# Optimization experiments

Hardware: AMD Instinct MI355X
Metric: run time of the kernel (lower is better)

Reference implementation:

```python
import jax, jax.numpy as jnp
import numpy as np
from jax import lax

B, CIN, IMG, K = 128, 3, 112, 7
C = 1024      # hidden_channels * channel_dilation
HID = 512     # hidden_channels
HW = (IMG // K) ** 2  # 256 patches
EPS = 1e-5


def _prelu(x, a):
    return jnp.where(x > 0, x, a * x)


def _bn(x, g, b):
    # BatchNorm2d with track_running_stats=False: always uses batch stats
    m = x.mean(axis=(0, 2, 3), keepdims=True)
    v = x.var(axis=(0, 2, 3), keepdims=True)
    return (x - m) * lax.rsqrt(v + EPS) * g[None, :, None, None] + b[None, :, None, None]


def setup_inputs() -> dict:
    key = jax.random.key(0)
    ks = jax.random.split(key, 16)
    d = {
        'x':  jax.random.normal(ks[0], (B, CIN, IMG, IMG), jnp.float32),
        'w0': jax.random.normal(ks[1], (C, CIN, K, K), jnp.float32) * 0.05,
        'b0': jax.random.normal(ks[2], (C,), jnp.float32) * 0.01,
        'a0': jnp.full((1,), 0.25, jnp.float32),
    }
    for i in range(1, 4):
        kw, kb = jax.random.split(jax.random.fold_in(key, i))
        d[f'w{i}'] = jax.random.normal(kw, (C, C), jnp.float32) * 0.02
        d[f'b{i}'] = jax.random.normal(kb, (C,), jnp.float32) * 0.01
        d[f'g{i}'] = jnp.ones((C,), jnp.float32)
        d[f'bt{i}'] = jnp.zeros((C,), jnp.float32)
        d[f'p{i}'] = jnp.full((1,), 0.25, jnp.float32)
    d['pos'] = jax.random.normal(ks[3], (1, HW, C), jnp.float32)
    d['am'] = jnp.full((1,), 0.25, jnp.float32)
    d['wm'] = jax.random.normal(ks[4], (HID, C), jnp.float32) * 0.03
    d['bm'] = jax.random.normal(ks[5], (HID,), jnp.float32) * 0.01
    pkeys = jax.random.split(ks[6], B)
    d['perm'] = jax.vmap(lambda k: jax.random.permutation(k, HW))(pkeys).astype(jnp.int32)
    return d


def reference(x, w0, b0, a0,
              w1, b1, g1, bt1, p1,
              w2, b2, g2, bt2, p2,
              w3, b3, g3, bt3, p3,
              pos, am, wm, bm, perm):
    # patch-embed conv: stride = kernel_size -> [B, C, 16, 16]
    h = lax.conv_general_dilated(x, w0, (K, K), 'VALID',
                                 dimension_numbers=('NCHW', 'OIHW', 'NCHW'))
    h = _prelu(h + b0[None, :, None, None], a0)
    for w, b, g, bt, p in ((w1, b1, g1, bt1, p1),
                           (w2, b2, g2, bt2, p2),
                           (w3, b3, g3, bt3, p3)):
        h = jnp.einsum('bchw,dc->bdhw', h, w) + b[None, :, None, None]  # 1x1 conv
        h = _prelu(_bn(h, g, bt), p)
    Bn, Cn, Hn, Wn = h.shape
    enc = h.reshape(Bn, Cn, Hn * Wn).transpose(0, 2, 1)  # [B, HW, C]
    enc = enc + pos                                      # private: add pos embedding
    enc = _prelu(enc, am) @ wm.T + bm                    # mixer -> [B, HW, HID]
    # private: per-sample token permutation (single batched gather)
    return jnp.take_along_axis(enc, perm[:, :, None], axis=1)
```

## Files before the change

kernel.cpp:

```cpp
#include <hip/hip_runtime.h>
#include <hip/hip_bf16.h>
#include <stdint.h>


typedef __attribute__((ext_vector_type(8))) short bf16x8;
typedef __attribute__((ext_vector_type(4))) float f32x4;

__device__ __forceinline__ float bf2f(uint32_t u) {
  union { uint32_t i; float f; } v; v.i = u << 16; return v.f;
}
__device__ __forceinline__ ushort f2bf(float f) {
  union { float f; uint32_t i; } v; v.f = f;
  uint32_t i = v.i;
  return (ushort)((i + 0x7FFFu + ((i >> 16) & 1u)) >> 16);
}

template<int EPI, int XB, int K, int DOUT>
__global__ void __launch_bounds__(512, 2)
gemm_kernel(const ushort* __restrict__ A, const ushort* __restrict__ Bw,
            const float* __restrict__ bias, const float* __restrict__ alpha,
            void* __restrict__ outp, float* __restrict__ part,
            const int* __restrict__ inv)
{
  __shared__ __align__(16) ushort At[2][256 * 64];
  __shared__ __align__(16) ushort Bt[2][256 * 64];
  const int tid  = threadIdx.x;
  const int lane = tid & 63;
  const int wid  = tid >> 6;
  const int wm   = wid >> 2;
  const int wn   = wid & 3;

  const int s = blockIdx.x;
  const int j = s >> 3;
  const int x = j & ((1 << XB) - 1);
  const int y = ((j >> XB) << 3) | (s & 7);
  const int t0 = y << 8;
  const int d0 = x << 8;

  f32x4 acc[8][4] = {};

  const int swz = (((lane >> 4) ^ (lane & 7)) << 4);
  const char* LA0 = (const char*)&At[0][0] + ((((wm << 7) + (lane & 15))) << 7) + swz;
  const char* LA1 = (const char*)&At[0][0] + ((((wm << 7) + (lane & 15))) << 7) + (swz ^ 64);
  const char* LB0 = (const char*)&Bt[0][0] + ((((wn << 6) + (lane & 15))) << 7) + swz;
  const char* LB1 = (const char*)&Bt[0][0] + ((((wn << 6) + (lane & 15))) << 7) + (swz ^ 64);

  const int lrow8 = lane >> 3;
  const int csrc  = (lane & 7) ^ lrow8;
  const ushort* gAw = A  + (size_t)(t0 + (wid << 4) + lrow8) * K + (csrc << 3);
  const ushort* gBw = Bw + (size_t)(d0 + (wid << 4) + lrow8) * K + (csrc << 3);
  char* stA = (char*)&At[0][0] + (wid << 11);
  char* stB = (char*)&Bt[0][0] + (wid << 11);

#define STAGE_A(T, BUF, H) do {                                                          \
    __builtin_amdgcn_global_load_lds(                                                    \
      (const __attribute__((address_space(1))) uint32_t*)(gAw + (size_t)((H)*128)*K + ((size_t)(T) << 6)),     \
      (__attribute__((address_space(3))) uint32_t*)(stA + (BUF)*32768 + (H)*16384), 16, 0, 0);                  \
    __builtin_amdgcn_global_load_lds(                                                    \
      (const __attribute__((address_space(1))) uint32_t*)(gAw + (size_t)((H)*128+8)*K + ((size_t)(T) << 6)),   \
      (__attribute__((address_space(3))) uint32_t*)(stA + (BUF)*32768 + (H)*16384 + 1024), 16, 0, 0);           \
  } while (0)
#define STAGE_B(T, BUF, H) do {                                                          \
    __builtin_amdgcn_global_load_lds(                                                    \
      (const __attribute__((address_space(1))) uint32_t*)(gBw + (size_t)((H)*128)*K + ((size_t)(T) << 6)),     \
      (__attribute__((address_space(3))) uint32_t*)(stB + (BUF)*32768 + (H)*16384), 16, 0, 0);                  \
    __builtin_amdgcn_global_load_lds(                                                    \
      (const __attribute__((address_space(1))) uint32_t*)(gBw + (size_t)((H)*128+8)*K + ((size_t)(T) << 6)),   \
      (__attribute__((address_space(3))) uint32_t*)(stB + (BUF)*32768 + (H)*16384 + 1024), 16, 0, 0);           \
  } while (0)

#define RD_A(dst, BASE, CUR, MH) do {                                                    \
    dst[0] = *(const bf16x8*)((BASE) + (CUR)*32768 + (MH)*8192 + 0);                     \
    dst[1] = *(const bf16x8*)((BASE) + (CUR)*32768 + (MH)*8192 + 2048);                  \
    dst[2] = *(const bf16x8*)((BASE) + (CUR)*32768 + (MH)*8192 + 4096);                  \
    dst[3] = *(const bf16x8*)((BASE) + (CUR)*32768 + (MH)*8192 + 6144);                  \
  } while (0)
#define RD_B(dst, BASE, CUR) do {                                                        \
    dst[0] = *(const bf16x8*)((BASE) + (CUR)*32768 + 0);                                 \
    dst[1] = *(const bf16x8*)((BASE) + (CUR)*32768 + 2048);                              \
    dst[2] = *(const bf16x8*)((BASE) + (CUR)*32768 + 4096);                              \
    dst[3] = *(const bf16x8*)((BASE) + (CUR)*32768 + 6144);                              \
  } while (0)
#define MFMA16(AF, BF, MH) do {                                                          \
    __builtin_amdgcn_s_setprio(1);                                                       \
    _Pragma("unroll")                                                                    \
    for (int m_ = 0; m_ < 4; ++m_)                                                       \
      _Pragma("unroll")                                                                  \
      for (int n_ = 0; n_ < 4; ++n_)                                                     \
        acc[((MH) << 2) + m_][n_] = __builtin_amdgcn_mfma_f32_16x16x32_bf16(             \
            AF[m_], BF[n_], acc[((MH) << 2) + m_][n_], 0, 0, 0);                         \
    __builtin_amdgcn_s_setprio(0);                                                       \
  } while (0)

#define TILE_BODY(T, CUR, HN1, HN2) do {                                                 \
                         \
    if (HN1) { asm volatile("s_waitcnt vmcnt(4)" ::: "memory"); }                        \
    else     { asm volatile("s_waitcnt vmcnt(0)" ::: "memory"); }                        \
    __builtin_amdgcn_s_barrier();                                                        \
                 \
    RD_B(b0f, LB0, CUR);                                                                 \
    RD_B(b1f, LB1, CUR);                                                                 \
    RD_A(aX, LA0, CUR, 0);                                                               \
    RD_A(aY, LA0, CUR, 1);                                                               \
    if (HN1) { STAGE_A((T) + 1, (CUR) ^ 1, 0); STAGE_A((T) + 1, (CUR) ^ 1, 1); }         \
    MFMA16(aX, b0f, 0);                                                                  \
    MFMA16(aY, b0f, 1);                                                                  \
                      \
    __builtin_amdgcn_s_barrier();                                                        \
                                                                           \
    if (HN2) { STAGE_B((T) + 2, CUR, 0); STAGE_B((T) + 2, CUR, 1); }                     \
    RD_A(aX, LA1, CUR, 0);                                                               \
    RD_A(aY, LA1, CUR, 1);                                                               \
    MFMA16(aX, b1f, 0);                                                                  \
    MFMA16(aY, b1f, 1);                                                                  \
  } while (0)

  constexpr int NT = K >> 6;

  STAGE_A(0, 0, 0); STAGE_A(0, 0, 1);
  STAGE_B(0, 0, 0); STAGE_B(0, 0, 1);
  STAGE_B(1, 1, 0); STAGE_B(1, 1, 1);

  bf16x8 aX[4], aY[4], b0f[4], b1f[4];

#pragma unroll 1
  for (int tp = 0; tp < NT; tp += 2) {
    const bool m1 = (tp + 2 < NT);
    TILE_BODY(tp,     0, true, m1);
    TILE_BODY(tp + 1, 1, m1, m1);
  }

  float bs[4];
#pragma unroll
  for (int n = 0; n < 4; ++n) bs[n] = bias[d0 + (wn << 6) + (n << 4) + (lane & 15)];
  float a0v = (EPI == 0) ? alpha[0] : 0.0f;
  float sA[4] = {0.f, 0.f, 0.f, 0.f}, s2A[4] = {0.f, 0.f, 0.f, 0.f};

#pragma unroll
  for (int m = 0; m < 8; ++m) {
#pragma unroll
    for (int r = 0; r < 4; ++r) {
      int row = t0 + (wm << 7) + (m << 4) + ((lane >> 4) << 2) + r;
      int orow = (EPI == 2) ? ((row & ~255) | inv[row]) : row;
#pragma unroll
      for (int n = 0; n < 4; ++n) {
        int d = d0 + (wn << 6) + (n << 4) + (lane & 15);
        float v = acc[m][n][r] + bs[n];
        if (EPI == 0) v = v > 0.f ? v : a0v * v;
        if (EPI == 1) { sA[n] += v; s2A[n] += v * v; }
        if (EPI == 2) ((float*)outp)[(size_t)orow * DOUT + d] = v;
        else          ((ushort*)outp)[(size_t)row * DOUT + d] = f2bf(v);
      }
    }
  }

  if (EPI == 1) {
    float2* sm = (float2*)&At[0][0];
    int slot = (wm << 2) | (lane >> 4);
    __syncthreads();
#pragma unroll
    for (int n = 0; n < 4; ++n) {
      int c = (wn << 6) + (n << 4) + (lane & 15);
      sm[slot * 256 + c] = make_float2(sA[n], s2A[n]);
    }
    __syncthreads();
    if (tid < 256) {
      float ss = 0.f, ss2 = 0.f;
      for (int q = 0; q < 8; ++q) {
        float2 v = sm[q * 256 + tid];
        ss += v.x; ss2 += v.y;
      }
      part[(size_t)y * 2048 + d0 + tid]        = ss;
      part[(size_t)y * 2048 + 1024 + d0 + tid] = ss2;
    }
  }
#undef STAGE_A
#undef STAGE_B
#undef RD_A
#undef RD_B
#undef MFMA16
#undef TILE_BODY
}

__global__ void bnfold_kernel(const float* __restrict__ part, const float* __restrict__ g,
                              const float* __restrict__ bt, float* __restrict__ scsh) {
  int d = (blockIdx.x << 8) + threadIdx.x;
  float s = 0.f, s2 = 0.f;
  for (int j = 0; j < 128; ++j) { s += part[j * 2048 + d]; s2 += part[j * 2048 + 1024 + d]; }
  float mean = s * (1.f / 32768.f);
  float var  = s2 * (1.f / 32768.f) - mean * mean;
  float sc = g[d] * rsqrtf(var + 1e-5f);
  scsh[d] = sc;
  scsh[1024 + d] = bt[d] - mean * sc;
}

template<bool MIX>
__global__ void bnact_kernel(ushort* __restrict__ Y, const float* __restrict__ scsh,
                             const float* __restrict__ p, const float* __restrict__ pos,
                             const float* __restrict__ am) {
  float pp = p[0];
  float aa = MIX ? am[0] : 0.f;
#pragma unroll 1
  for (int it = 0; it < 8; ++it) {
    size_t vi = ((size_t)it << 19) + ((size_t)blockIdx.x << 8) + threadIdx.x;
    size_t i = vi << 3;
    int d = (int)(i & 1023);
    float pv[8];
    if (MIX) {
      int prow = (int)((i >> 10) & 255);
      const float4* pb = (const float4*)(pos + ((size_t)prow << 10) + d);
      float4 pA = pb[0], pB = pb[1];
      pv[0]=pA.x; pv[1]=pA.y; pv[2]=pA.z; pv[3]=pA.w;
      pv[4]=pB.x; pv[5]=pB.y; pv[6]=pB.z; pv[7]=pB.w;
    }
    uint4 raw = *(const uint4*)(Y + i);
    uint32_t w[4] = {raw.x, raw.y, raw.z, raw.w};
    uint32_t o[4];
#pragma unroll
    for (int q = 0; q < 4; ++q) {
      int dd = d + q * 2;
      float v0 = bf2f(w[q] & 0xFFFFu) * scsh[dd]     + scsh[1024 + dd];
      float v1 = bf2f(w[q] >> 16)     * scsh[dd + 1] + scsh[1024 + dd + 1];
      v0 = v0 > 0.f ? v0 : pp * v0;
      v1 = v1 > 0.f ? v1 : pp * v1;
      if (MIX) {
        v0 += pv[2 * q];     v1 += pv[2 * q + 1];
        v0 = v0 > 0.f ? v0 : aa * v0;
        v1 = v1 > 0.f ? v1 : aa * v1;
      }
      o[q] = (uint32_t)f2bf(v0) | ((uint32_t)f2bf(v1) << 16);
    }
    *(uint4*)(Y + i) = make_uint4(o[0], o[1], o[2], o[3]);
  }
}

__global__ void prep_kernel(const float* __restrict__ x,
                            const float* __restrict__ w0, const float* __restrict__ w1,
                            const float* __restrict__ w2, const float* __restrict__ w3,
                            const float* __restrict__ wm, const int* __restrict__ perm,
                            ushort* __restrict__ P, ushort* __restrict__ w0b,
                            ushort* __restrict__ w1b, ushort* __restrict__ w2b,
                            ushort* __restrict__ w3b, ushort* __restrict__ wmb,
                            int* __restrict__ inv) {
  const int b = blockIdx.x, tid = threadIdx.x;
  if (b < 2048) {
    int t0 = b << 4;
#pragma unroll 1
    for (int tt = 0; tt < 16; ++tt) {
      int t = t0 + tt;
      ushort v = 0;
      if (tid < 147) {
        int bb = t >> 8, pidx = t & 255;
        int pi = pidx >> 4, pj = pidx & 15;
        int cin = tid / 49, rem = tid - cin * 49;
        int dy = rem / 7, dx = rem - dy * 7;
        v = f2bf(x[(size_t)(bb * 3 + cin) * 12544 + (size_t)(pi * 7 + dy) * 112 + (pj * 7 + dx)]);
      }
      P[(size_t)t * 256 + tid] = v;
    }
  } else if (b < 4096) {
    int i = ((b - 2048) << 8) + tid;
#pragma unroll
    for (int r = 0; r < 2; ++r) {
      int idx = (r << 19) + i;
      w1b[idx] = f2bf(w1[idx]);
      w2b[idx] = f2bf(w2[idx]);
      w3b[idx] = f2bf(w3[idx]);
    }
    wmb[i] = f2bf(wm[i]);
  } else if (b < 4224) {
    int t = ((b - 4096) << 8) + tid;
    inv[(t & ~255) + perm[t]] = t & 255;
  } else {
    int d = b - 4224;
    w0b[d * 256 + tid] = (tid < 147) ? f2bf(w0[d * 147 + tid]) : (ushort)0;
  }
}

extern "C" void kernel_launch(void* const* d_in, const int* in_sizes, int n_in,
                              void* d_out, int out_size, void* d_ws, size_t ws_size,
                              hipStream_t stream) {
  const float* x   = (const float*)d_in[0];
  const float* w0  = (const float*)d_in[1];
  const float* b0  = (const float*)d_in[2];
  const float* a0  = (const float*)d_in[3];
  const float* w1  = (const float*)d_in[4];
  const float* b1  = (const float*)d_in[5];
  const float* g1  = (const float*)d_in[6];
  const float* bt1 = (const float*)d_in[7];
  const float* p1  = (const float*)d_in[8];
  const float* w2  = (const float*)d_in[9];
  const float* b2  = (const float*)d_in[10];
  const float* g2  = (const float*)d_in[11];
  const float* bt2 = (const float*)d_in[12];
  const float* p2  = (const float*)d_in[13];
  const float* w3  = (const float*)d_in[14];
  const float* b3  = (const float*)d_in[15];
  const float* g3  = (const float*)d_in[16];
  const float* bt3 = (const float*)d_in[17];
  const float* p3  = (const float*)d_in[18];
  const float* pos = (const float*)d_in[19];
  const float* am  = (const float*)d_in[20];
  const float* wm  = (const float*)d_in[21];
  const float* bm  = (const float*)d_in[22];
  const int*  perm = (const int*)d_in[23];

  char* ws = (char*)d_ws;
  ushort* B0   = (ushort*)ws;
  ushort* B1   = (ushort*)(ws + 67108864);
  float*  part = (float*)(ws + 134217728);
  float*  scsh = (float*)(ws + 134217728 + 2097152);
  int*    inv  = (int*)  (ws + 134217728 + 2097152 + 8192);
  char*   wb   = ws + 134217728 + 2097152 + 8192 + 131072;
  ushort* w1b  = (ushort*)wb;
  ushort* w2b  = w1b + 1048576;
  ushort* w3b  = w2b + 1048576;
  ushort* wmb  = w3b + 1048576;
  ushort* w0b  = wmb + 524288;

  prep_kernel<<<dim3(5248), dim3(256), 0, stream>>>(
      x, w0, w1, w2, w3, wm, perm, B1, w0b, w1b, w2b, w3b, wmb, inv);

  gemm_kernel<0, 2, 256, 1024><<<dim3(512), dim3(512), 0, stream>>>(
      B1, w0b, b0, a0, (void*)B0, nullptr, nullptr);

  gemm_kernel<1, 2, 1024, 1024><<<dim3(512), dim3(512), 0, stream>>>(
      B0, w1b, b1, nullptr, (void*)B1, part, nullptr);
  bnfold_kernel<<<dim3(4), dim3(256), 0, stream>>>(part, g1, bt1, scsh);
  bnact_kernel<false><<<dim3(2048), dim3(256), 0, stream>>>(B1, scsh, p1, nullptr, nullptr);

  gemm_kernel<1, 2, 1024, 1024><<<dim3(512), dim3(512), 0, stream>>>(
      B1, w2b, b2, nullptr, (void*)B0, part, nullptr);
  bnfold_kernel<<<dim3(4), dim3(256), 0, stream>>>(part, g2, bt2, scsh);
  bnact_kernel<false><<<dim3(2048), dim3(256), 0, stream>>>(B0, scsh, p2, nullptr, nullptr);

  gemm_kernel<1, 2, 1024, 1024><<<dim3(512), dim3(512), 0, stream>>>(
      B0, w3b, b3, nullptr, (void*)B1, part, nullptr);
  bnfold_kernel<<<dim3(4), dim3(256), 0, stream>>>(part, g3, bt3, scsh);
  bnact_kernel<true><<<dim3(2048), dim3(256), 0, stream>>>(B1, scsh, p3, pos, am);

  gemm_kernel<2, 1, 1024, 512><<<dim3(256), dim3(512), 0, stream>>>(
      B1, wmb, bm, nullptr, d_out, nullptr, inv);
}
```

Measured before the change: 396.3 us.

## Triple-buffer B tiles in LDS to drop the mid-tile barrier

Adds a third LDS buffer for the B operand and rotates read, next and stage indices, so B for tile T+2 can be staged right after the single barrier instead of behind a second one. The wait becomes a full vmcnt(0) at each tile start, and A and B fragment reads are interleaved with the MFMAs. LDS use per block grows from 128 KB to 160 KB, which may limit occupancy (launch bounds ask for 2 blocks per CU). Waiting on all loads each tile may also expose more memory latency.

```diff
diff --git a/kernel.cpp b/kernel.cpp
--- a/kernel.cpp
+++ b/kernel.cpp
@@ -23,7 +23,7 @@
             const int* __restrict__ inv)
 {
   __shared__ __align__(16) ushort At[2][256 * 64];
-  __shared__ __align__(16) ushort Bt[2][256 * 64];
+  __shared__ __align__(16) ushort Bt[3][256 * 64];
   const int tid  = threadIdx.x;
   const int lane = tid & 63;
   const int wid  = tid >> 6;
@@ -60,13 +60,13 @@
       (const __attribute__((address_space(1))) uint32_t*)(gAw + (size_t)((H)*128+8)*K + ((size_t)(T) << 6)),   \
       (__attribute__((address_space(3))) uint32_t*)(stA + (BUF)*32768 + (H)*16384 + 1024), 16, 0, 0);           \
   } while (0)
-#define STAGE_B(T, BUF, H) do {                                                          \
+#define STAGE_B(T, BOFF, H) do {                                                         \
     __builtin_amdgcn_global_load_lds(                                                    \
       (const __attribute__((address_space(1))) uint32_t*)(gBw + (size_t)((H)*128)*K + ((size_t)(T) << 6)),     \
-      (__attribute__((address_space(3))) uint32_t*)(stB + (BUF)*32768 + (H)*16384), 16, 0, 0);                  \
+      (__attribute__((address_space(3))) uint32_t*)(stB + (BOFF) + (H)*16384), 16, 0, 0);                       \
     __builtin_amdgcn_global_load_lds(                                                    \
       (const __attribute__((address_space(1))) uint32_t*)(gBw + (size_t)((H)*128+8)*K + ((size_t)(T) << 6)),   \
-      (__attribute__((address_space(3))) uint32_t*)(stB + (BUF)*32768 + (H)*16384 + 1024), 16, 0, 0);           \
+      (__attribute__((address_space(3))) uint32_t*)(stB + (BOFF) + (H)*16384 + 1024), 16, 0, 0);                \
   } while (0)
 
 #define RD_A(dst, BASE, CUR, MH) do {                                                    \
@@ -75,11 +75,11 @@
     dst[2] = *(const bf16x8*)((BASE) + (CUR)*32768 + (MH)*8192 + 4096);                  \
     dst[3] = *(const bf16x8*)((BASE) + (CUR)*32768 + (MH)*8192 + 6144);                  \
   } while (0)
-#define RD_B(dst, BASE, CUR) do {                                                        \
-    dst[0] = *(const bf16x8*)((BASE) + (CUR)*32768 + 0);                                 \
-    dst[1] = *(const bf16x8*)((BASE) + (CUR)*32768 + 2048);                              \
-    dst[2] = *(const bf16x8*)((BASE) + (CUR)*32768 + 4096);                              \
-    dst[3] = *(const bf16x8*)((BASE) + (CUR)*32768 + 6144);                              \
+#define RD_B(dst, BASE, BOFF) do {                                                       \
+    dst[0] = *(const bf16x8*)((BASE) + (BOFF) + 0);                                      \
+    dst[1] = *(const bf16x8*)((BASE) + (BOFF) + 2048);                                   \
+    dst[2] = *(const bf16x8*)((BASE) + (BOFF) + 4096);                                   \
+    dst[3] = *(const bf16x8*)((BASE) + (BOFF) + 6144);                                   \
   } while (0)
 #define MFMA16(AF, BF, MH) do {                                                          \
     __builtin_amdgcn_s_setprio(1);                                                       \
@@ -93,34 +93,30 @@
   } while (0)
 
 #define TILE_BODY(T, CUR, HN1, HN2) do {                                                 \
-                         \
-    if (HN1) { asm volatile("s_waitcnt vmcnt(4)" ::: "memory"); }                        \
-    else     { asm volatile("s_waitcnt vmcnt(0)" ::: "memory"); }                        \
+    asm volatile("s_waitcnt vmcnt(0)" ::: "memory");                                     \
     __builtin_amdgcn_s_barrier();                                                        \
-                 \
-    RD_B(b0f, LB0, CUR);                                                                 \
-    RD_B(b1f, LB1, CUR);                                                                 \
     RD_A(aX, LA0, CUR, 0);                                                               \
+    RD_B(b0f, LB0, bR);                                                                  \
+    if (HN1) { STAGE_A((T) + 1, (CUR) ^ 1, 0); STAGE_A((T) + 1, (CUR) ^ 1, 1); }         \
+    if (HN2) { STAGE_B((T) + 2, bS, 0); STAGE_B((T) + 2, bS, 1); }                       \
+    MFMA16(aX, b0f, 0);                                                                  \
     RD_A(aY, LA0, CUR, 1);                                                               \
-    if (HN1) { STAGE_A((T) + 1, (CUR) ^ 1, 0); STAGE_A((T) + 1, (CUR) ^ 1, 1); }         \
-    MFMA16(aX, b0f, 0);                                                                  \
     MFMA16(aY, b0f, 1);                                                                  \
-                      \
-    __builtin_amdgcn_s_barrier();                                                        \
-                                                                           \
-    if (HN2) { STAGE_B((T) + 2, CUR, 0); STAGE_B((T) + 2, CUR, 1); }                     \
     RD_A(aX, LA1, CUR, 0);                                                               \
+    RD_B(b1f, LB1, bR);                                                                  \
+    MFMA16(aX, b1f, 0);                                                                  \
     RD_A(aY, LA1, CUR, 1);                                                               \
-    MFMA16(aX, b1f, 0);                                                                  \
     MFMA16(aY, b1f, 1);                                                                  \
+    { int tmp_ = bR; bR = bN; bN = bS; bS = tmp_; }                                      \
   } while (0)
 
   constexpr int NT = K >> 6;
 
   STAGE_A(0, 0, 0); STAGE_A(0, 0, 1);
   STAGE_B(0, 0, 0); STAGE_B(0, 0, 1);
-  STAGE_B(1, 1, 0); STAGE_B(1, 1, 1);
-
+  STAGE_B(1, 32768, 0); STAGE_B(1, 32768, 1);
+
+  int bR = 0, bN = 32768, bS = 65536;
   bf16x8 aX[4], aY[4], b0f[4], b1f[4];
 
 #pragma unroll 1
```

Measured after the change: 386.7 us. 1.02x faster.
